# Optimization experiments

Hardware: AMD Instinct MI355X
Metric: run time of the kernel (lower is better)

## Reference

```python
import jax, jax.numpy as jnp
import numpy as np

B, H, Wd, D, NC = 8, 64, 128, 272, 19   # batch, H/16, W/16, capsule feat dim, num_classes
P, NI = 524288, 4096                    # total points, total instances


def setup_inputs() -> dict:
    key = jax.random.key(0)
    k0, k1, k2, k3 = jax.random.split(key, 4)
    return {
        "class_capsules": jax.random.normal(k0, (B, H, Wd, D), dtype=jnp.float32),
        "W": jax.random.normal(k1, (D, NC), dtype=jnp.float32) * 0.05,
        "b": jnp.zeros((NC,), dtype=jnp.float32),
        "point_idx": jax.random.randint(k2, (P,), 0, B * H * Wd, dtype=jnp.int32),
        "segment_ids": jnp.sort(jax.random.randint(k3, (P,), 0, NI, dtype=jnp.int32)),
        "num_segments": NI,
    }


def reference(class_capsules, W, b, point_idx, segment_ids, num_segments):
    # Batched version of: inst_capsules = class_capsules[i, ys, xs, :];
    # pooled = mean(inst_capsules, 0); out = sigmoid(linear(pooled))
    # point_idx are flat (already deduped) indices into the [B*H*Wd] grid.
    feats = class_capsules.reshape(-1, class_capsules.shape[-1])[point_idx]        # [P, D]
    sums = jax.ops.segment_sum(feats, segment_ids, num_segments=num_segments)       # [NI, D]
    counts = jax.ops.segment_sum(jnp.ones((feats.shape[0],), feats.dtype),
                                 segment_ids, num_segments=num_segments)            # [NI]
    pooled = sums / jnp.maximum(counts, 1.0)[:, None]                                # mean pool
    return jax.nn.sigmoid(pooled @ W + b)                                            # [NI, NC]
```

## Files before the change

kernel.cpp:

```cpp
#include <hip/hip_runtime.h>
#include <math.h>

#define NROWS 65536
#define DD    272
#define NC    19
#define NP    524288
#define NSEG  4096
#define PS    20

__global__ __launch_bounds__(256) void proj_kernel(
    const float* __restrict__ X, const float* __restrict__ W,
    float* __restrict__ proj) {
  const int t    = threadIdx.x;
  const int lane = t & 63;
  const int q    = __builtin_amdgcn_readfirstlane(t >> 6);
  const int row0 = blockIdx.x * 64;

  __shared__ float Xs[64 * 17];
  __shared__ float R[4 * 64 * NC];

  float acc[NC];
#pragma unroll
  for (int c = 0; c < NC; ++c) acc[c] = 0.f;

  const int r_ld = t >> 2;
  const int c4   = t & 3;
  const float* gsrc = X + (size_t)(row0 + r_ld) * DD + c4 * 4;

  for (int chunk = 0; chunk < 17; ++chunk) {
    float4 v = *(const float4*)(gsrc + chunk * 16);
    __syncthreads();
    float* dst = &Xs[r_ld * 17 + c4 * 4];
    dst[0] = v.x; dst[1] = v.y; dst[2] = v.z; dst[3] = v.w;
    __syncthreads();
    const int d0 = chunk * 16;
#pragma unroll
    for (int k = 0; k < 4; ++k) {
      const int c16 = q + 4 * k;
      const float x = Xs[lane * 17 + c16];
      const float* wr = W + (d0 + c16) * NC;
#pragma unroll
      for (int c = 0; c < NC; ++c) acc[c] = fmaf(x, wr[c], acc[c]);
    }
  }

#pragma unroll
  for (int c = 0; c < NC; ++c) R[(q * 64 + lane) * NC + c] = acc[c];
  __syncthreads();
#pragma unroll
  for (int j = 0; j < 5; ++j) {
    int f = t + 256 * j;
    int r = f / PS;
    int c = f % PS;
    float s = 0.f;
    if (c < NC) {
      s = R[r * NC + c] + R[(64 + r) * NC + c] +
          R[(128 + r) * NC + c] + R[(192 + r) * NC + c];
    }
    proj[(size_t)row0 * PS + f] = s;
  }
}

__global__ __launch_bounds__(64) void pool_kernel(
    const float* __restrict__ proj, const int* __restrict__ point_idx,
    const int* __restrict__ seg, const float* __restrict__ bias,
    float* __restrict__ out) {
  const int s    = blockIdx.x;
  const int lane = threadIdx.x;

  int lo = 0, hi = NP;
  while (lo < hi) { int mid = (lo + hi) >> 1; if (seg[mid] <  s) lo = mid + 1; else hi = mid; }
  const int start = lo;
  hi = NP;
  while (lo < hi) { int mid = (lo + hi) >> 1; if (seg[mid] <= s) lo = mid + 1; else hi = mid; }
  const int end = lo;

  float a[PS];
#pragma unroll
  for (int j = 0; j < PS; ++j) a[j] = 0.f;

  for (int p = start + lane; p < end; p += 64) {
    const int pi = point_idx[p];
    const float4* row = (const float4*)(proj + (size_t)pi * PS);
#pragma unroll
    for (int j = 0; j < 5; ++j) {
      float4 v = row[j];
      a[4 * j + 0] += v.x; a[4 * j + 1] += v.y;
      a[4 * j + 2] += v.z; a[4 * j + 3] += v.w;
    }
  }

#pragma unroll
  for (int off = 32; off > 0; off >>= 1) {
#pragma unroll
    for (int j = 0; j < NC; ++j) a[j] += __shfl_xor(a[j], off);
  }

  if (lane == 0) {
    const float inv = 1.f / fmaxf((float)(end - start), 1.f);
#pragma unroll
    for (int c = 0; c < NC; ++c) {
      float m = a[c] * inv + bias[c];
      out[s * NC + c] = 1.f / (1.f + expf(-m));
    }
  }
}

__global__ __launch_bounds__(256) void fallback_kernel(
    const float* __restrict__ X, const float* __restrict__ W,
    const float* __restrict__ bias, const int* __restrict__ point_idx,
    const int* __restrict__ seg, float* __restrict__ out) {
  const int s = blockIdx.x;
  const int t = threadIdx.x;
  __shared__ float Ps[DD];

  int lo = 0, hi = NP;
  while (lo < hi) { int mid = (lo + hi) >> 1; if (seg[mid] <  s) lo = mid + 1; else hi = mid; }
  const int start = lo;
  hi = NP;
  while (lo < hi) { int mid = (lo + hi) >> 1; if (seg[mid] <= s) lo = mid + 1; else hi = mid; }
  const int end = lo;

  float a0 = 0.f, a1 = 0.f;
  for (int p = start; p < end; ++p) {
    const int pi = point_idx[p];
    const float* row = X + (size_t)pi * DD;
    a0 += row[t];
    if (t < DD - 256) a1 += row[256 + t];
  }
  const float inv = 1.f / fmaxf((float)(end - start), 1.f);
  Ps[t] = a0 * inv;
  if (t < DD - 256) Ps[256 + t] = a1 * inv;
  __syncthreads();

  if (t < NC) {
    float acc = bias[t];
    for (int d = 0; d < DD; ++d) acc = fmaf(Ps[d], W[d * NC + t], acc);
    out[s * NC + t] = 1.f / (1.f + expf(-acc));
  }
}

extern "C" void kernel_launch(void* const* d_in, const int* in_sizes, int n_in,
                              void* d_out, int out_size, void* d_ws, size_t ws_size,
                              hipStream_t stream) {
  const float* X         = (const float*)d_in[0];
  const float* W         = (const float*)d_in[1];
  const float* bias      = (const float*)d_in[2];
  const int*   point_idx = (const int*)d_in[3];
  const int*   seg       = (const int*)d_in[4];
  float*       out       = (float*)d_out;

  const size_t need = (size_t)NROWS * PS * sizeof(float);
  if (ws_size >= need) {
    float* proj = (float*)d_ws;
    proj_kernel<<<NROWS / 64, 256, 0, stream>>>(X, W, proj);
    pool_kernel<<<NSEG, 64, 0, stream>>>(proj, point_idx, seg, bias, out);
  } else {
    fallback_kernel<<<NSEG, 256, 0, stream>>>(X, W, bias, point_idx, seg, out);
  }
}
```

Before: 141.5 us.

## Precompute segment boundaries in projection kernel and prefetch next X chunk

Extra blocks appended to the projection launch scan the sorted segment ids and write a start-offset table for every segment. The pool kernel then reads its start and end from that table instead of running two binary searches over the full point array. The projection loop also loads the next 16-column chunk of X into a register before computing on the current one, so the global load overlaps the FMA work. The cost is a little extra workspace and more blocks in the first launch.

```diff
diff --git a/kernel.cpp b/kernel.cpp
--- a/kernel.cpp
+++ b/kernel.cpp
@@ -8,10 +8,26 @@
 #define NSEG  4096
 #define PS    20
 
-__global__ __launch_bounds__(256) void proj_kernel(
+#define PROJ_BLOCKS   (NROWS / 64)
+#define BOUND_BLOCKS  (NP / 256)
+
+__global__ __launch_bounds__(256) void proj_bounds_kernel(
     const float* __restrict__ X, const float* __restrict__ W,
-    float* __restrict__ proj) {
-  const int t    = threadIdx.x;
+    const int* __restrict__ seg, float* __restrict__ proj,
+    int* __restrict__ bnd) {
+  const int t = threadIdx.x;
+
+  if (blockIdx.x >= PROJ_BLOCKS) {
+    const int p = (blockIdx.x - PROJ_BLOCKS) * 256 + t;
+    const int cur  = seg[p];
+    const int prev = (p == 0) ? -1 : seg[p - 1];
+    for (int s = prev + 1; s <= cur; ++s) bnd[s] = p;
+    if (p == NP - 1) {
+      for (int s = cur + 1; s <= NSEG; ++s) bnd[s] = NP;
+    }
+    return;
+  }
+
   const int lane = t & 63;
   const int q    = __builtin_amdgcn_readfirstlane(t >> 6);
   const int row0 = blockIdx.x * 64;
@@ -27,12 +43,15 @@
   const int c4   = t & 3;
   const float* gsrc = X + (size_t)(row0 + r_ld) * DD + c4 * 4;
 
+  float4 v = *(const float4*)gsrc;
+
   for (int chunk = 0; chunk < 17; ++chunk) {
-    float4 v = *(const float4*)(gsrc + chunk * 16);
     __syncthreads();
     float* dst = &Xs[r_ld * 17 + c4 * 4];
     dst[0] = v.x; dst[1] = v.y; dst[2] = v.z; dst[3] = v.w;
     __syncthreads();
+    if (chunk < 16)
+      v = *(const float4*)(gsrc + (chunk + 1) * 16);
     const int d0 = chunk * 16;
 #pragma unroll
     for (int k = 0; k < 4; ++k) {
@@ -63,17 +82,12 @@
 
 __global__ __launch_bounds__(64) void pool_kernel(
     const float* __restrict__ proj, const int* __restrict__ point_idx,
-    const int* __restrict__ seg, const float* __restrict__ bias,
+    const int* __restrict__ bnd, const float* __restrict__ bias,
     float* __restrict__ out) {
   const int s    = blockIdx.x;
   const int lane = threadIdx.x;
-
-  int lo = 0, hi = NP;
-  while (lo < hi) { int mid = (lo + hi) >> 1; if (seg[mid] <  s) lo = mid + 1; else hi = mid; }
-  const int start = lo;
-  hi = NP;
-  while (lo < hi) { int mid = (lo + hi) >> 1; if (seg[mid] <= s) lo = mid + 1; else hi = mid; }
-  const int end = lo;
+  const int start = bnd[s];
+  const int end   = bnd[s + 1];
 
   float a[PS];
 #pragma unroll
@@ -150,11 +164,14 @@
   const int*   seg       = (const int*)d_in[4];
   float*       out       = (float*)d_out;
 
-  const size_t need = (size_t)NROWS * PS * sizeof(float);
+  const size_t proj_bytes = (size_t)NROWS * PS * sizeof(float);
+  const size_t need = proj_bytes + (size_t)(NSEG + 1) * sizeof(int);
   if (ws_size >= need) {
     float* proj = (float*)d_ws;
-    proj_kernel<<<NROWS / 64, 256, 0, stream>>>(X, W, proj);
-    pool_kernel<<<NSEG, 64, 0, stream>>>(proj, point_idx, seg, bias, out);
+    int*   bnd  = (int*)((char*)d_ws + proj_bytes);
+    proj_bounds_kernel<<<PROJ_BLOCKS + BOUND_BLOCKS, 256, 0, stream>>>(
+        X, W, seg, proj, bnd);
+    pool_kernel<<<NSEG, 64, 0, stream>>>(proj, point_idx, bnd, bias, out);
   } else {
     fallback_kernel<<<NSEG, 256, 0, stream>>>(X, W, bias, point_idx, seg, out);
   }
```

Measured after the change: 128.7 us. -9.1%, faster.
